# Performance work log

Measured on AMD Instinct MI355X. Metric: run time of the kernel, lower is better.

The kernel has to match this reference:

```python
import jax, jax.numpy as jnp
import numpy as np

INV_SQRT2 = 0.7071067811865476  # 1/sqrt(2), orthonormal Haar
N_LEVELS = 3


def setup_inputs() -> dict:
    key = jax.random.key(0)
    ks = jax.random.split(key, 5)
    B, S, D = 16, 4096, 512
    x = jax.random.normal(ks[0], (B, S, D), dtype=jnp.float32)
    sizes = [256, 128, 64]  # detail-band sizes for 3-level DWT of 512
    Wd0 = jax.random.normal(ks[1], (sizes[0], sizes[0]), dtype=jnp.float32) * 0.02
    Wd1 = jax.random.normal(ks[2], (sizes[1], sizes[1]), dtype=jnp.float32) * 0.02
    Wd2 = jax.random.normal(ks[3], (sizes[2], sizes[2]), dtype=jnp.float32) * 0.02
    Wa = jax.random.normal(ks[4], (sizes[2], sizes[2]), dtype=jnp.float32) * 0.02
    return {
        'x': x,
        'Wd0': Wd0, 'bd0': jnp.zeros((sizes[0],), jnp.float32),
        'Wd1': Wd1, 'bd1': jnp.zeros((sizes[1],), jnp.float32),
        'Wd2': Wd2, 'bd2': jnp.zeros((sizes[2],), jnp.float32),
        'Wa': Wa, 'ba': jnp.zeros((sizes[2],), jnp.float32),
    }


def reference(x, Wd0, bd0, Wd1, bd1, Wd2, bd2, Wa, ba):
    # Multi-level Haar DWT along the feature axis.
    details = []
    a = x
    for _ in range(N_LEVELS):
        e = a[..., 0::2]
        o = a[..., 1::2]
        details.append((e - o) * INV_SQRT2)  # detail coefficients
        a = (e + o) * INV_SQRT2              # approximation coefficients

    # Per-level small linear transforms (torch Linear: y = x @ W.T + b).
    Wds, bds = [Wd0, Wd1, Wd2], [bd0, bd1, bd2]
    details = [details[i] @ Wds[i].T + bds[i] for i in range(N_LEVELS)]
    a = a @ Wa.T + ba

    # Inverse Haar DWT (orthonormal): even=(a+d)/sqrt2, odd=(a-d)/sqrt2, interleave.
    for i in reversed(range(N_LEVELS)):
        d = details[i]
        e = (a + d) * INV_SQRT2
        o = (a - d) * INV_SQRT2
        a = jnp.stack([e, o], axis=-1).reshape(a.shape[:-1] + (a.shape[-1] * 2,))
    return a
```

## Files before the change

kernel.cpp:

```cpp
#include <hip/hip_runtime.h>
#include <stdint.h>

typedef float  f32x4  __attribute__((ext_vector_type(4)));
typedef short  bf16x8 __attribute__((ext_vector_type(8)));
typedef int    i32x4  __attribute__((ext_vector_type(4)));

#define C1f 0.70710678118654752f
#define C2f 0.5f
#define C3f 0.35355339059327373f

#define NT 512
#define CH 16
#define RBF 2064
#define CHSZ (CH*RBF)
#define NBUF 4
#define RPB 256
#define NCHUNK (RPB/CH)

__device__ __forceinline__ unsigned int f2b(float f) {
    unsigned int u; __builtin_memcpy(&u, &f, 4);
    u += 0x7fffu + ((u >> 16) & 1u);
    return u >> 16;
}
__device__ __forceinline__ unsigned int pack2(float lo, float hi) {
    return f2b(lo) | (f2b(hi) << 16);
}
__device__ __forceinline__ bf16x8 cast8(i32x4 v) {
    bf16x8 r; __builtin_memcpy(&r, &v, 16); return r;
}
__device__ __forceinline__ unsigned int cvtpk(float lo, float hi) {
    unsigned int r;
    asm("v_cvt_pk_bf16_f32 %0, %1, %2" : "=v"(r) : "v"(lo), "v"(hi));
    return r;
}

__device__ __forceinline__ void lds_barrier() {
    asm volatile("s_waitcnt lgkmcnt(0)" ::: "memory");
    __builtin_amdgcn_s_barrier();
    __builtin_amdgcn_sched_barrier(0);
}
__device__ __forceinline__ void vwait4() { asm volatile("s_waitcnt vmcnt(4)" ::: "memory"); __builtin_amdgcn_sched_barrier(0); }
__device__ __forceinline__ void vwait6() { asm volatile("s_waitcnt vmcnt(6)" ::: "memory"); __builtin_amdgcn_sched_barrier(0); }
__device__ __forceinline__ void vwait8() { asm volatile("s_waitcnt vmcnt(8)" ::: "memory"); __builtin_amdgcn_sched_barrier(0); }

__device__ __forceinline__ void gld_lds16(const float* g, char* l) {
    __builtin_amdgcn_global_load_lds((const unsigned int*)g, (unsigned int*)l, 16, 0, 0);
}

__device__ __forceinline__ bf16x8 g_frag(int o, int i0,
        const float* __restrict__ W0, const float* __restrict__ W1,
        const float* __restrict__ W2, const float* __restrict__ Wa)
{
    const float s0o = (o & 1) ? -1.f : 1.f;
    const float s1o = ((o >> 1) & 1) ? -1.f : 1.f;
    const float s2o = ((o >> 2) & 1) ? -1.f : 1.f;
    const float4 w0 = *(const float4*)(W0 + (o >> 1) * 256 + (i0 >> 1));
    const float2 w1 = *(const float2*)(W1 + (o >> 2) * 128 + (i0 >> 2));
    const float  w2 = W2[(o >> 3) * 64 + (i0 >> 3)];
    const float  wa = Wa[(o >> 3) * 64 + (i0 >> 3)];
    const float base = 0.125f * wa;
    const float c2   = 0.125f * s2o * w2;
    const float c1   = 0.25f  * s1o;
    const float c0   = 0.5f   * s0o;
    const float w0a[4] = { w0.x, w0.y, w0.z, w0.w };
    const float w1a[2] = { w1.x, w1.y };
    float g[8];
    #pragma unroll
    for (int e = 0; e < 8; ++e) {
        const float t2 = ((e >> 2) & 1) ? -c2 : c2;
        const float t1 = (((e >> 1) & 1) ? -c1 : c1) * w1a[e >> 2];
        const float t0 = ((e & 1) ? -c0 : c0) * w0a[e >> 1];
        g[e] = base + t2 + t1 + t0;
    }
    i32x4 p = { (int)pack2(g[0],g[1]), (int)pack2(g[2],g[3]),
                (int)pack2(g[4],g[5]), (int)pack2(g[6],g[7]) };
    return cast8(p);
}

__global__ void prep(const float* __restrict__ W0, const float* __restrict__ b0,
                     const float* __restrict__ W1, const float* __restrict__ b1,
                     const float* __restrict__ W2, const float* __restrict__ b2,
                     const float* __restrict__ Wa, const float* __restrict__ ba,
                     unsigned short* __restrict__ ws)
{
    const int gid  = blockIdx.x * 256 + threadIdx.x;
    const int blob = gid >> 6, lane = gid & 63;
    const int otg  = blob >> 4, ks = blob & 15;
    const int o  = otg * 16 + (lane & 15);
    const int i0 = ks * 32 + ((lane >> 4) * 8);
    bf16x8 f = g_frag(o, i0, W0, W1, W2, Wa);
    i32x4 p; __builtin_memcpy(&p, &f, 16);
    *(i32x4*)(ws + blob * 512 + lane * 8) = p;
    if (gid < 512) {
        float* gv = (float*)(ws + 262144);
        const int oo = gid;
        const float s0 = (oo & 1) ? -C1f : C1f;
        const float s1 = ((oo >> 1) & 1) ? -C2f : C2f;
        const float s2 = ((oo >> 2) & 1) ? -C3f : C3f;
        gv[oo] = C3f * ba[oo >> 3] + s2 * b2[oo >> 3] + s1 * b1[oo >> 2] + s0 * b0[oo >> 1];
    }
}

template<int USE_WS>
__global__ __launch_bounds__(NT, 2)
void wavelet_gemm(const float* __restrict__ x,
                  const float* __restrict__ W0, const float* __restrict__ b0,
                  const float* __restrict__ W1, const float* __restrict__ b1,
                  const float* __restrict__ W2, const float* __restrict__ b2,
                  const float* __restrict__ Wa, const float* __restrict__ ba,
                  const unsigned short* __restrict__ wsb,
                  float* __restrict__ out, int nblk)
{
    __shared__ char lds[NBUF * CHSZ];

    const int tid  = threadIdx.x;
    const int lane = tid & 63;
    const int wave = tid >> 6;

    const int cpx = nblk >> 3;
    const int lbid = ((int)blockIdx.x & 7) * cpx + ((int)blockIdx.x >> 3);
    const int chalf = lbid & 1;
    const long rowblk = (long)(lbid >> 1) * RPB;

    const int otg0 = chalf * 16 + wave * 2;
    const int col0 = otg0 * 16;
    const int bc0  = col0 + ((lane >> 4) << 2);

    bf16x8 B0[16], B1[16];
    if (USE_WS) {
        #pragma unroll
        for (int ks = 0; ks < 16; ++ks) {
            B0[ks] = cast8(*(const i32x4*)(wsb + ((size_t)(otg0 * 16 + ks) * 512) + lane * 8));
            B1[ks] = cast8(*(const i32x4*)(wsb + ((size_t)((otg0 + 1) * 16 + ks) * 512) + lane * 8));
        }
    } else {
        #pragma unroll
        for (int ks = 0; ks < 16; ++ks) {
            B0[ks] = g_frag(col0 + (lane & 15),      ks * 32 + ((lane >> 4) * 8), W0, W1, W2, Wa);
            B1[ks] = g_frag(col0 + 16 + (lane & 15), ks * 32 + ((lane >> 4) * 8), W0, W1, W2, Wa);
        }
    }
    #pragma unroll
    for (int ks = 0; ks < 16; ++ks) {
        i32x4 t0, t1;
        __builtin_memcpy(&t0, &B0[ks], 16);
        __builtin_memcpy(&t1, &B1[ks], 16);
        asm volatile("" : "+v"(t0), "+v"(t1));
        __builtin_memcpy(&B0[ks], &t0, 16);
        __builtin_memcpy(&B1[ks], &t1, 16);
    }

    f32x4 gv40, gv41;
    if (USE_WS) {
        const float4 g0 = *(const float4*)((const float*)(wsb + 262144) + bc0);
        const float4 g1 = *(const float4*)((const float*)(wsb + 262144) + bc0 + 16);
        gv40 = f32x4{ g0.x, g0.y, g0.z, g0.w };
        gv41 = f32x4{ g1.x, g1.y, g1.z, g1.w };
    } else {
        #pragma unroll
        for (int j = 0; j < 4; ++j) {
            #pragma unroll
            for (int t = 0; t < 2; ++t) {
                const int col = bc0 + t * 16 + j;
                const float s0 = (col & 1) ? -C1f : C1f;
                const float s1 = ((col >> 1) & 1) ? -C2f : C2f;
                const float s2 = ((col >> 2) & 1) ? -C3f : C3f;
                const float v = C3f * ba[col >> 3] + s2 * b2[col >> 3] + s1 * b1[col >> 2] + s0 * b0[col >> 1];
                if (t == 0) gv40[j] = v; else gv41[j] = v;
            }
        }
    }

    auto stage = [&](int c) {
        char* base = lds + (c & (NBUF - 1)) * CHSZ;
        const float* xc = x + (rowblk + (long)c * CH) * 512;
        #pragma unroll
        for (int i = 0; i < 2; ++i) {
            const int r = wave * 2 + i;
            const float* gp = xc + (long)r * 512 + lane * 4;
            char* lp = base + r * RBF;
            gld_lds16(gp, lp);
            gld_lds16(gp + 256, lp + 1024);
        }
        __builtin_amdgcn_sched_barrier(0);
    };
    auto compute = [&](int c) {
        const char* pa = lds + (c & (NBUF - 1)) * CHSZ + (lane & 15) * RBF + ((lane >> 4) * 32);
        f32x4 acc0 = {}, acc1 = {};
        #pragma unroll
        for (int ks = 0; ks < 16; ++ks) {
            f32x4 lo = *(const f32x4*)(pa + ks * 128);
            f32x4 hi = *(const f32x4*)(pa + ks * 128 + 16);
            i32x4 pk = { (int)cvtpk(lo[0], lo[1]), (int)cvtpk(lo[2], lo[3]),
                         (int)cvtpk(hi[0], hi[1]), (int)cvtpk(hi[2], hi[3]) };
            bf16x8 a = cast8(pk);
            acc0 = __builtin_amdgcn_mfma_f32_16x16x32_bf16(B0[ks], a, acc0, 0, 0, 0);
            acc1 = __builtin_amdgcn_mfma_f32_16x16x32_bf16(B1[ks], a, acc1, 0, 0, 0);
        }
        const long rr = (rowblk + (long)c * CH + (lane & 15)) * 512;
        *(f32x4*)(out + rr + bc0)      = acc0 + gv40;
        *(f32x4*)(out + rr + bc0 + 16) = acc1 + gv41;
    };

    stage(0);
    stage(1);
    vwait4();
    lds_barrier();

    #pragma unroll 1
    for (int c = 0; c < NCHUNK; ++c) {
        if (c + 2 < NCHUNK) stage(c + 2);
        compute(c);
        if (c + 2 < NCHUNK) {
            if (c == 0) vwait6(); else vwait8();
            lds_barrier();
        } else if (c + 1 < NCHUNK) {
            vwait4();
            lds_barrier();
        }
    }
}

extern "C" void kernel_launch(void* const* d_in, const int* in_sizes, int n_in,
                              void* d_out, int out_size, void* d_ws, size_t ws_size,
                              hipStream_t stream)
{
    const float* x  = (const float*)d_in[0];
    const float* W0 = (const float*)d_in[1];
    const float* b0 = (const float*)d_in[2];
    const float* W1 = (const float*)d_in[3];
    const float* b1 = (const float*)d_in[4];
    const float* W2 = (const float*)d_in[5];
    const float* b2 = (const float*)d_in[6];
    const float* Wa = (const float*)d_in[7];
    const float* ba = (const float*)d_in[8];
    float* out = (float*)d_out;

    const int nrows = in_sizes[0] / 512;
    const int nblk  = (nrows / RPB) * 2;

    if (ws_size >= (size_t)(524288 + 2048)) {
        unsigned short* ws = (unsigned short*)d_ws;
        prep<<<128, 256, 0, stream>>>(W0, b0, W1, b1, W2, b2, Wa, ba, ws);
        wavelet_gemm<1><<<nblk, NT, 0, stream>>>(x, W0, b0, W1, b1, W2, b2, Wa, ba, ws, out, nblk);
    } else {
        wavelet_gemm<0><<<nblk, NT, 0, stream>>>(x, W0, b0, W1, b1, W2, b2, Wa, ba, nullptr, out, nblk);
    }
}
```

Before: 75.79 us.

## Drop LDS staging; load activations directly from global with register prefetch

Removes the LDS ring buffer, global_load_lds staging and block barriers, and instead has each wave read its A-fragments straight from global memory into registers with a four-step rolling prefetch. Blocks shrink to 256 threads and the output columns are split across four column groups instead of two, so there are twice as many blocks. Each x row is now read by four blocks instead of two, which raises global or L2 traffic, and the uncoalesced per-lane 32-byte loads may cost more than the removed synchronisation saves.

```diff
diff --git a/kernel.cpp b/kernel.cpp
--- a/kernel.cpp
+++ b/kernel.cpp
@@ -9,13 +9,10 @@
 #define C2f 0.5f
 #define C3f 0.35355339059327373f
 
-#define NT 512
-#define CH 16
-#define RBF 2064
-#define CHSZ (CH*RBF)
-#define NBUF 4
+#define NT 256
 #define RPB 256
-#define NCHUNK (RPB/CH)
+#define NCOLG 4
+#define NMT (RPB/16)
 
 __device__ __forceinline__ unsigned int f2b(float f) {
     unsigned int u; __builtin_memcpy(&u, &f, 4);
@@ -32,19 +29,6 @@
     unsigned int r;
     asm("v_cvt_pk_bf16_f32 %0, %1, %2" : "=v"(r) : "v"(lo), "v"(hi));
     return r;
-}
-
-__device__ __forceinline__ void lds_barrier() {
-    asm volatile("s_waitcnt lgkmcnt(0)" ::: "memory");
-    __builtin_amdgcn_s_barrier();
-    __builtin_amdgcn_sched_barrier(0);
-}
-__device__ __forceinline__ void vwait4() { asm volatile("s_waitcnt vmcnt(4)" ::: "memory"); __builtin_amdgcn_sched_barrier(0); }
-__device__ __forceinline__ void vwait6() { asm volatile("s_waitcnt vmcnt(6)" ::: "memory"); __builtin_amdgcn_sched_barrier(0); }
-__device__ __forceinline__ void vwait8() { asm volatile("s_waitcnt vmcnt(8)" ::: "memory"); __builtin_amdgcn_sched_barrier(0); }
-
-__device__ __forceinline__ void gld_lds16(const float* g, char* l) {
-    __builtin_amdgcn_global_load_lds((const unsigned int*)g, (unsigned int*)l, 16, 0, 0);
 }
 
 __device__ __forceinline__ bf16x8 g_frag(int o, int i0,
@@ -111,18 +95,16 @@
                   const unsigned short* __restrict__ wsb,
                   float* __restrict__ out, int nblk)
 {
-    __shared__ char lds[NBUF * CHSZ];
-
     const int tid  = threadIdx.x;
     const int lane = tid & 63;
     const int wave = tid >> 6;
 
     const int cpx = nblk >> 3;
     const int lbid = ((int)blockIdx.x & 7) * cpx + ((int)blockIdx.x >> 3);
-    const int chalf = lbid & 1;
-    const long rowblk = (long)(lbid >> 1) * RPB;
-
-    const int otg0 = chalf * 16 + wave * 2;
+    const int colg = lbid & (NCOLG - 1);
+    const long rowblk = (long)(lbid >> 2) * RPB;
+
+    const int otg0 = colg * 8 + wave * 2;
     const int col0 = otg0 * 16;
     const int bc0  = col0 + ((lane >> 4) << 2);
 
@@ -171,53 +153,34 @@
         }
     }
 
-    auto stage = [&](int c) {
-        char* base = lds + (c & (NBUF - 1)) * CHSZ;
-        const float* xc = x + (rowblk + (long)c * CH) * 512;
-        #pragma unroll
-        for (int i = 0; i < 2; ++i) {
-            const int r = wave * 2 + i;
-            const float* gp = xc + (long)r * 512 + lane * 4;
-            char* lp = base + r * RBF;
-            gld_lds16(gp, lp);
-            gld_lds16(gp + 256, lp + 1024);
-        }
-        __builtin_amdgcn_sched_barrier(0);
-    };
-    auto compute = [&](int c) {
-        const char* pa = lds + (c & (NBUF - 1)) * CHSZ + (lane & 15) * RBF + ((lane >> 4) * 32);
+    const char* xb = (const char*)(x + rowblk * 512) + (lane & 15) * 2048 + ((lane >> 4) * 32);
+
+    #pragma unroll 1
+    for (int mt = 0; mt < NMT; ++mt) {
+        const char* xa = xb + (long)mt * 16 * 2048;
+        f32x4 lo[4], hi[4];
+        #pragma unroll
+        for (int p = 0; p < 4; ++p) {
+            lo[p] = *(const f32x4*)(xa + p * 128);
+            hi[p] = *(const f32x4*)(xa + p * 128 + 16);
+        }
         f32x4 acc0 = {}, acc1 = {};
         #pragma unroll
         for (int ks = 0; ks < 16; ++ks) {
-            f32x4 lo = *(const f32x4*)(pa + ks * 128);
-            f32x4 hi = *(const f32x4*)(pa + ks * 128 + 16);
-            i32x4 pk = { (int)cvtpk(lo[0], lo[1]), (int)cvtpk(lo[2], lo[3]),
-                         (int)cvtpk(hi[0], hi[1]), (int)cvtpk(hi[2], hi[3]) };
+            f32x4 l = lo[ks & 3], h = hi[ks & 3];
+            if (ks + 4 < 16) {
+                lo[ks & 3] = *(const f32x4*)(xa + (ks + 4) * 128);
+                hi[ks & 3] = *(const f32x4*)(xa + (ks + 4) * 128 + 16);
+            }
+            i32x4 pk = { (int)cvtpk(l[0], l[1]), (int)cvtpk(l[2], l[3]),
+                         (int)cvtpk(h[0], h[1]), (int)cvtpk(h[2], h[3]) };
             bf16x8 a = cast8(pk);
             acc0 = __builtin_amdgcn_mfma_f32_16x16x32_bf16(B0[ks], a, acc0, 0, 0, 0);
             acc1 = __builtin_amdgcn_mfma_f32_16x16x32_bf16(B1[ks], a, acc1, 0, 0, 0);
         }
-        const long rr = (rowblk + (long)c * CH + (lane & 15)) * 512;
+        const long rr = (rowblk + (long)mt * 16 + (lane & 15)) * 512;
         *(f32x4*)(out + rr + bc0)      = acc0 + gv40;
         *(f32x4*)(out + rr + bc0 + 16) = acc1 + gv41;
-    };
-
-    stage(0);
-    stage(1);
-    vwait4();
-    lds_barrier();
-
-    #pragma unroll 1
-    for (int c = 0; c < NCHUNK; ++c) {
-        if (c + 2 < NCHUNK) stage(c + 2);
-        compute(c);
-        if (c + 2 < NCHUNK) {
-            if (c == 0) vwait6(); else vwait8();
-            lds_barrier();
-        } else if (c + 1 < NCHUNK) {
-            vwait4();
-            lds_barrier();
-        }
     }
 }
 
@@ -237,7 +200,7 @@
     float* out = (float*)d_out;
 
     const int nrows = in_sizes[0] / 512;
-    const int nblk  = (nrows / RPB) * 2;
+    const int nblk  = (nrows / RPB) * NCOLG;
 
     if (ws_size >= (size_t)(524288 + 2048)) {
         unsigned short* ws = (unsigned short*)d_ws;
```

New measurement: 298.0 us. 293% more time.
